# Kernel optimization log

Hardware: AMD Instinct MI355X
Metric: run time of the kernel (lower is better)

Reference implementation:

```python
import jax, jax.numpy as jnp
import numpy as np

N_EDGES = 100000      # hyperedge table rows
N_INC = 2000000       # incidences (rows of hyper_node)
D_E = 64              # edge_in_channels
D_N = 64              # node_in_channels
D_OUT = 64            # node_out_channels


def setup_inputs() -> dict:
    key = jax.random.key(0)
    k1, k2, k3, k4 = jax.random.split(key, 4)
    hyperedge = jax.random.normal(k1, (N_EDGES, D_E), dtype=jnp.float32)
    hyper_node = jax.random.normal(k2, (N_INC, D_N), dtype=jnp.float32)
    ve_affiliation = jax.random.randint(k3, (2, N_INC), 0, N_EDGES, dtype=jnp.int64)
    # Linear weight stored torch-style [out, in]; xavier-ish scale
    W = jax.random.normal(k4, (D_OUT, D_E * 2 + D_N), dtype=jnp.float32) * 0.05
    b = jnp.zeros((D_OUT,), dtype=jnp.float32)
    return {"hyperedge": hyperedge, "hyper_node": hyper_node,
            "ve_affiliation": ve_affiliation, "W": W, "b": b}


def reference(hyperedge, hyper_node, ve_affiliation, W, b):
    # gather edge features for both endpoints of each incidence
    edge_i = hyperedge[ve_affiliation[0]]          # [N_INC, D_E]
    edge_j = hyperedge[ve_affiliation[1]]          # [N_INC, D_E]
    x = jnp.concatenate((edge_i, edge_j, hyper_node), axis=-1)  # [N_INC, 2*D_E+D_N]
    h = x @ W.T + b                                # [N_INC, D_OUT]
    return jax.nn.relu(h)
```

## Files before the change

kernel.cpp:

```cpp
#include <hip/hip_runtime.h>


typedef __bf16 bf16x8 __attribute__((ext_vector_type(8)));
typedef float  f32x4  __attribute__((ext_vector_type(4)));

static __device__ __forceinline__ bf16x8 cvt8(f32x4 a, f32x4 b) {
  bf16x8 r;
  r[0] = (__bf16)a[0]; r[1] = (__bf16)a[1]; r[2] = (__bf16)a[2]; r[3] = (__bf16)a[3];
  r[4] = (__bf16)b[0]; r[5] = (__bf16)b[1]; r[6] = (__bf16)b[2]; r[7] = (__bf16)b[3];
  return r;
}

static __device__ __forceinline__ bf16x8 load_frag(const float* __restrict__ p) {
  f32x4 a = *(const f32x4*)p;
  f32x4 b = *(const f32x4*)(p + 4);
  return cvt8(a, b);
}

#define N_EDGES  100000
#define N_INC    2000000
#define N_TILES  (N_INC / 16)
#define E_TILES  (N_EDGES / 16)

__global__ __launch_bounds__(256, 2) void edge_proj(
    const float* __restrict__ hyperedge,
    const float* __restrict__ W,
    const float* __restrict__ bias,
    float*       __restrict__ proj)
{
  const int lane = threadIdx.x & 63;
  const int wid  = (blockIdx.x * blockDim.x + threadIdx.x) >> 6;
  if (wid >= E_TILES) return;
  const int m    = lane & 15;
  const int quad = lane >> 4;
  const int koff = quad * 8;

  bf16x8 Wf[8][2];
  #pragma unroll
  for (int t = 0; t < 8; ++t) {
    const float* wr = W + (long)((t & 3) * 16 + m) * 192 + (t >> 2) * 64 + koff;
    #pragma unroll
    for (int f = 0; f < 2; ++f)
      Wf[t][f] = load_frag(wr + f * 32);
  }

  const int ebase = wid * 16;
  const float* er = hyperedge + (long)(ebase + m) * 64 + koff;
  bf16x8 hef0 = load_frag(er);
  bf16x8 hef1 = load_frag(er + 32);

  f32x4 acc[8] = { {0,0,0,0},{0,0,0,0},{0,0,0,0},{0,0,0,0},
                   {0,0,0,0},{0,0,0,0},{0,0,0,0},{0,0,0,0} };
  #pragma unroll
  for (int t = 0; t < 8; ++t) {
    acc[t] = __builtin_amdgcn_mfma_f32_16x16x32_bf16(Wf[t][0], hef0, acc[t], 0, 0, 0);
    acc[t] = __builtin_amdgcn_mfma_f32_16x16x32_bf16(Wf[t][1], hef1, acc[t], 0, 0, 0);
  }

  float* pr = proj + (long)(ebase + m) * 128 + quad * 4;
  #pragma unroll
  for (int t = 0; t < 8; ++t) {
    f32x4 v = acc[t];
    if (t < 4) {
      f32x4 bv = *(const f32x4*)(bias + t * 16 + quad * 4);
      v[0] += bv[0]; v[1] += bv[1]; v[2] += bv[2]; v[3] += bv[3];
    }
    *(f32x4*)(pr + t * 16) = v;
  }
}

__global__ __launch_bounds__(256, 4) void e2v_gather(
    const float* __restrict__ hyper_node,
    const int*   __restrict__ aff,
    const float* __restrict__ W,
    const float* __restrict__ proj,
    float*       __restrict__ out)
{
  const int lane = threadIdx.x & 63;
  const int wid  = (blockIdx.x * blockDim.x + threadIdx.x) >> 6;
  const int nw   = (gridDim.x * blockDim.x) >> 6;
  const int m    = lane & 15;
  const int quad = lane >> 4;
  const int koff = quad * 8;

  bf16x8 Wf2[4][2];
  #pragma unroll
  for (int t = 0; t < 4; ++t) {
    const float* wr = W + (long)(t * 16 + m) * 192 + 128 + koff;
    #pragma unroll
    for (int f = 0; f < 2; ++f)
      Wf2[t][f] = load_frag(wr + f * 32);
  }

  const int* __restrict__ aff0 = aff;
  const int* __restrict__ aff1 = aff + N_INC;

  int tile = wid;
  if (tile >= N_TILES) return;

  int ni0 = aff0[tile * 16 + m];
  int ni1 = aff1[tile * 16 + m];

  for (; tile < N_TILES; tile += nw) {
    const int i0 = ni0;
    const int i1 = ni1;
    const int nb = tile * 16;

    const int nt = tile + nw;
    if (nt < N_TILES) {
      ni0 = aff0[nt * 16 + m];
      ni1 = aff1[nt * 16 + m];
    }

    const float* p0 = proj + (long)i0 * 128 + quad * 4;
    const float* p1 = proj + (long)i1 * 128 + 64 + quad * 4;
    f32x4 g0[4], g1[4];
    #pragma unroll
    for (int t = 0; t < 4; ++t) {
      g0[t] = *(const f32x4*)(p0 + t * 16);
      g1[t] = *(const f32x4*)(p1 + t * 16);
    }

    const float* nd = hyper_node + (long)(nb + m) * 64 + koff;
    bf16x8 Nf0 = load_frag(nd);
    bf16x8 Nf1 = load_frag(nd + 32);

    f32x4 acc[4] = { {0,0,0,0},{0,0,0,0},{0,0,0,0},{0,0,0,0} };
    #pragma unroll
    for (int t = 0; t < 4; ++t)
      acc[t] = __builtin_amdgcn_mfma_f32_16x16x32_bf16(Wf2[t][0], Nf0, acc[t], 0, 0, 0);
    #pragma unroll
    for (int t = 0; t < 4; ++t)
      acc[t] = __builtin_amdgcn_mfma_f32_16x16x32_bf16(Wf2[t][1], Nf1, acc[t], 0, 0, 0);

    float* op = out + (long)(nb + m) * 64 + quad * 4;
    #pragma unroll
    for (int t = 0; t < 4; ++t) {
      f32x4 v;
      #pragma unroll
      for (int r = 0; r < 4; ++r) {
        float x = acc[t][r] + g0[t][r] + g1[t][r];
        v[r] = x > 0.f ? x : 0.f;
      }
      *(f32x4*)(op + t * 16) = v;
    }
  }
}

__global__ __launch_bounds__(256, 2) void e2v_mfma(
    const float* __restrict__ hyperedge,
    const float* __restrict__ hyper_node,
    const int*   __restrict__ aff,
    const float* __restrict__ W,
    const float* __restrict__ bias,
    float*       __restrict__ out)
{
  const int lane = threadIdx.x & 63;
  const int wid  = (blockIdx.x * blockDim.x + threadIdx.x) >> 6;
  const int nw   = (gridDim.x * blockDim.x) >> 6;
  const int m    = lane & 15;
  const int quad = lane >> 4;
  const int koff = quad * 8;

  bf16x8 Bf[4][6];
  #pragma unroll
  for (int t = 0; t < 4; ++t) {
    const float* wr = W + (t * 16 + m) * 192 + koff;
    #pragma unroll
    for (int f = 0; f < 6; ++f)
      Bf[t][f] = load_frag(wr + f * 32);
  }
  float bv[4];
  #pragma unroll
  for (int t = 0; t < 4; ++t) bv[t] = bias[t * 16 + m];

  const int* __restrict__ aff0 = aff;
  const int* __restrict__ aff1 = aff + N_INC;

  for (int tile = wid; tile < N_TILES; tile += nw) {
    const int n_base = tile * 16;
    const int i0 = aff0[n_base + m];
    const int i1 = aff1[n_base + m];
    const float* e0 = hyperedge  + (long)i0 * 64 + koff;
    const float* e1 = hyperedge  + (long)i1 * 64 + koff;
    const float* nd = hyper_node + (long)(n_base + m) * 64 + koff;

    bf16x8 A[6];
    A[0] = load_frag(e0);
    A[1] = load_frag(e0 + 32);
    A[2] = load_frag(e1);
    A[3] = load_frag(e1 + 32);
    A[4] = load_frag(nd);
    A[5] = load_frag(nd + 32);

    f32x4 acc[4] = { {0.f,0.f,0.f,0.f}, {0.f,0.f,0.f,0.f},
                     {0.f,0.f,0.f,0.f}, {0.f,0.f,0.f,0.f} };
    #pragma unroll
    for (int f = 0; f < 6; ++f) {
      #pragma unroll
      for (int t = 0; t < 4; ++t)
        acc[t] = __builtin_amdgcn_mfma_f32_16x16x32_bf16(A[f], Bf[t][f], acc[t], 0, 0, 0);
    }

    #pragma unroll
    for (int t = 0; t < 4; ++t) {
      const int o = t * 16 + m;
      #pragma unroll
      for (int r = 0; r < 4; ++r) {
        const int inc = n_base + quad * 4 + r;
        float v = acc[t][r] + bv[t];
        out[(long)inc * 64 + o] = v > 0.f ? v : 0.f;
      }
    }
  }
}

extern "C" void kernel_launch(void* const* d_in, const int* in_sizes, int n_in,
                              void* d_out, int out_size, void* d_ws, size_t ws_size,
                              hipStream_t stream) {
  const float* hyperedge  = (const float*)d_in[0];
  const float* hyper_node = (const float*)d_in[1];
  const int*   aff        = (const int*)d_in[2];
  const float* W          = (const float*)d_in[3];
  const float* bias       = (const float*)d_in[4];
  float* out = (float*)d_out;

  const size_t need = (size_t)N_EDGES * 128 * sizeof(float);
  if (ws_size >= need) {
    float* proj = (float*)d_ws;
    hipLaunchKernelGGL(edge_proj, dim3((E_TILES * 64 + 255) / 256), dim3(256), 0, stream,
                       hyperedge, W, bias, proj);
    hipLaunchKernelGGL(e2v_gather, dim3(4096), dim3(256), 0, stream,
                       hyper_node, aff, W, proj, out);
  } else {
    hipLaunchKernelGGL(e2v_mfma, dim3(4096), dim3(256), 0, stream,
                       hyperedge, hyper_node, aff, W, bias, out);
  }
}
```

Measured before the change: 989.9 us.

## Process two tiles per wave iteration with nontemporal streaming loads and stores

The gather kernel now handles a pair of 16-row incidence tiles per loop iteration, issuing all gathered projection loads and node loads for both tiles before computing, which raises memory-level parallelism. Streaming data (affiliation indices, hyper_node rows, output) uses nontemporal loads and stores so that it does not evict the reused projection table from cache. The gathered projections now seed the MFMA accumulators instead of being added afterwards. The cost is higher register pressure, which may reduce occupancy.

```diff
diff --git a/kernel.cpp b/kernel.cpp
--- a/kernel.cpp
+++ b/kernel.cpp
@@ -17,9 +17,16 @@
   return cvt8(a, b);
 }
 
+static __device__ __forceinline__ bf16x8 load_frag_nt(const float* __restrict__ p) {
+  f32x4 a = __builtin_nontemporal_load((const f32x4*)p);
+  f32x4 b = __builtin_nontemporal_load((const f32x4*)(p + 4));
+  return cvt8(a, b);
+}
+
 #define N_EDGES  100000
 #define N_INC    2000000
 #define N_TILES  (N_INC / 16)
+#define P_TILES  (N_TILES / 2)
 #define E_TILES  (N_EDGES / 16)
 
 __global__ __launch_bounds__(256, 2) void edge_proj(
@@ -95,54 +102,84 @@
   const int* __restrict__ aff0 = aff;
   const int* __restrict__ aff1 = aff + N_INC;
 
-  int tile = wid;
-  if (tile >= N_TILES) return;
-
-  int ni0 = aff0[tile * 16 + m];
-  int ni1 = aff1[tile * 16 + m];
-
-  for (; tile < N_TILES; tile += nw) {
-    const int i0 = ni0;
-    const int i1 = ni1;
-    const int nb = tile * 16;
-
-    const int nt = tile + nw;
-    if (nt < N_TILES) {
-      ni0 = aff0[nt * 16 + m];
-      ni1 = aff1[nt * 16 + m];
-    }
-
-    const float* p0 = proj + (long)i0 * 128 + quad * 4;
-    const float* p1 = proj + (long)i1 * 128 + 64 + quad * 4;
-    f32x4 g0[4], g1[4];
-    #pragma unroll
-    for (int t = 0; t < 4; ++t) {
-      g0[t] = *(const f32x4*)(p0 + t * 16);
-      g1[t] = *(const f32x4*)(p1 + t * 16);
-    }
-
-    const float* nd = hyper_node + (long)(nb + m) * 64 + koff;
-    bf16x8 Nf0 = load_frag(nd);
-    bf16x8 Nf1 = load_frag(nd + 32);
-
-    f32x4 acc[4] = { {0,0,0,0},{0,0,0,0},{0,0,0,0},{0,0,0,0} };
-    #pragma unroll
-    for (int t = 0; t < 4; ++t)
-      acc[t] = __builtin_amdgcn_mfma_f32_16x16x32_bf16(Wf2[t][0], Nf0, acc[t], 0, 0, 0);
-    #pragma unroll
-    for (int t = 0; t < 4; ++t)
-      acc[t] = __builtin_amdgcn_mfma_f32_16x16x32_bf16(Wf2[t][1], Nf1, acc[t], 0, 0, 0);
-
-    float* op = out + (long)(nb + m) * 64 + quad * 4;
-    #pragma unroll
-    for (int t = 0; t < 4; ++t) {
-      f32x4 v;
-      #pragma unroll
-      for (int r = 0; r < 4; ++r) {
-        float x = acc[t][r] + g0[t][r] + g1[t][r];
-        v[r] = x > 0.f ? x : 0.f;
-      }
-      *(f32x4*)(op + t * 16) = v;
+  int p = wid;
+  if (p >= P_TILES) return;
+
+  long pba = (long)p * 32 + m;
+  int ci_a0 = __builtin_nontemporal_load(aff0 + pba);
+  int ci_b0 = __builtin_nontemporal_load(aff0 + pba + 16);
+  int ci_a1 = __builtin_nontemporal_load(aff1 + pba);
+  int ci_b1 = __builtin_nontemporal_load(aff1 + pba + 16);
+
+  for (; p < P_TILES; p += nw) {
+    const int ia0 = ci_a0, ia1 = ci_a1, ib0 = ci_b0, ib1 = ci_b1;
+    const int nb = p * 32;
+
+    const int np = p + nw;
+    if (np < P_TILES) {
+      const long pb = (long)np * 32 + m;
+      ci_a0 = __builtin_nontemporal_load(aff0 + pb);
+      ci_b0 = __builtin_nontemporal_load(aff0 + pb + 16);
+      ci_a1 = __builtin_nontemporal_load(aff1 + pb);
+      ci_b1 = __builtin_nontemporal_load(aff1 + pb + 16);
+    }
+
+    const float* pa0 = proj + (long)ia0 * 128 + quad * 4;
+    const float* pa1 = proj + (long)ia1 * 128 + 64 + quad * 4;
+    const float* pb0 = proj + (long)ib0 * 128 + quad * 4;
+    const float* pb1 = proj + (long)ib1 * 128 + 64 + quad * 4;
+    f32x4 ga0[4], ga1[4], gb0[4], gb1[4];
+    #pragma unroll
+    for (int t = 0; t < 4; ++t) {
+      ga0[t] = *(const f32x4*)(pa0 + t * 16);
+      ga1[t] = *(const f32x4*)(pa1 + t * 16);
+      gb0[t] = *(const f32x4*)(pb0 + t * 16);
+      gb1[t] = *(const f32x4*)(pb1 + t * 16);
+    }
+
+    const float* nda = hyper_node + (long)(nb + m) * 64 + koff;
+    const float* ndb = nda + 16 * 64;
+    bf16x8 Na0 = load_frag_nt(nda);
+    bf16x8 Na1 = load_frag_nt(nda + 32);
+    bf16x8 Nb0 = load_frag_nt(ndb);
+    bf16x8 Nb1 = load_frag_nt(ndb + 32);
+
+    f32x4 acca[4];
+    #pragma unroll
+    for (int t = 0; t < 4; ++t) acca[t] = ga0[t] + ga1[t];
+    #pragma unroll
+    for (int t = 0; t < 4; ++t)
+      acca[t] = __builtin_amdgcn_mfma_f32_16x16x32_bf16(Wf2[t][0], Na0, acca[t], 0, 0, 0);
+    #pragma unroll
+    for (int t = 0; t < 4; ++t)
+      acca[t] = __builtin_amdgcn_mfma_f32_16x16x32_bf16(Wf2[t][1], Na1, acca[t], 0, 0, 0);
+
+    float* opa = out + (long)(nb + m) * 64 + quad * 4;
+    #pragma unroll
+    for (int t = 0; t < 4; ++t) {
+      f32x4 v = acca[t];
+      #pragma unroll
+      for (int r = 0; r < 4; ++r) v[r] = v[r] > 0.f ? v[r] : 0.f;
+      __builtin_nontemporal_store(v, (f32x4*)(opa + t * 16));
+    }
+
+    f32x4 accb[4];
+    #pragma unroll
+    for (int t = 0; t < 4; ++t) accb[t] = gb0[t] + gb1[t];
+    #pragma unroll
+    for (int t = 0; t < 4; ++t)
+      accb[t] = __builtin_amdgcn_mfma_f32_16x16x32_bf16(Wf2[t][0], Nb0, accb[t], 0, 0, 0);
+    #pragma unroll
+    for (int t = 0; t < 4; ++t)
+      accb[t] = __builtin_amdgcn_mfma_f32_16x16x32_bf16(Wf2[t][1], Nb1, accb[t], 0, 0, 0);
+
+    float* opb = opa + 16 * 64;
+    #pragma unroll
+    for (int t = 0; t < 4; ++t) {
+      f32x4 v = accb[t];
+      #pragma unroll
+      for (int r = 0; r < 4; ++r) v[r] = v[r] > 0.f ? v[r] : 0.f;
+      __builtin_nontemporal_store(v, (f32x4*)(opb + t * 16));
     }
   }
 }
```

After: 1.042 ms. 5.2% more time.
